# Kernel optimization log

Measured on AMD Instinct MI355X. Metric: run time of the kernel, lower is better.

The kernel has to match this reference:

```python
import jax, jax.numpy as jnp
import numpy as np

B, N, C = 2, 2048, 768
H, HD = 12, 64
HID = 3072
LN_EPS = 1e-5
POL_EPS = 1e-6


def _layer_norm(x, g, b):
    m = jnp.mean(x, axis=-1, keepdims=True)
    v = jnp.mean(jnp.square(x - m), axis=-1, keepdims=True)
    return (x - m) * jax.lax.rsqrt(v + LN_EPS) * g + b


def _softmax_with_policy(attn, policy):
    # attn: [B,H,N,N], policy: [B,N,1]
    n = attn.shape[-1]
    ap = policy.reshape(policy.shape[0], 1, 1, n)  # [B,1,1,N]
    eye = jnp.eye(n, dtype=ap.dtype)[None, None]   # [1,1,N,N]
    ap = ap + (1.0 - ap) * eye                     # always attend to self
    attn = attn - jnp.max(attn, axis=-1, keepdims=True)
    attn = jnp.exp(attn.astype(jnp.float32)) * ap.astype(jnp.float32)
    attn = (attn + POL_EPS / n) / (jnp.sum(attn, axis=-1, keepdims=True) + POL_EPS)
    return attn


def setup_inputs() -> dict:
    key = jax.random.key(0)
    ks = jax.random.split(key, 12)
    s = lambda fan_in: 1.0 / np.sqrt(fan_in)
    x = jax.random.normal(ks[0], (B, N, C), dtype=jnp.float32)
    policy = (jax.random.uniform(ks[1], (B, N, 1)) > 0.5).astype(jnp.float32)
    return {
        "x": x,
        "policy": policy,
        "ln1_g": jnp.ones((C,), jnp.float32),
        "ln1_b": jnp.zeros((C,), jnp.float32),
        "qkv_w": jax.random.uniform(ks[2], (3 * H * HD, C), jnp.float32, -s(C), s(C)),
        "proj_w": jax.random.uniform(ks[3], (C, H * HD), jnp.float32, -s(H * HD), s(H * HD)),
        "proj_b": jnp.zeros((C,), jnp.float32),
        "ln2_g": jnp.ones((C,), jnp.float32),
        "ln2_b": jnp.zeros((C,), jnp.float32),
        "fc1_w": jax.random.uniform(ks[4], (HID, C), jnp.float32, -s(C), s(C)),
        "fc1_b": jnp.zeros((HID,), jnp.float32),
        "fc2_w": jax.random.uniform(ks[5], (C, HID), jnp.float32, -s(HID), s(HID)),
        "fc2_b": jnp.zeros((C,), jnp.float32),
    }


def reference(x, policy, ln1_g, ln1_b, qkv_w, proj_w, proj_b, ln2_g, ln2_b, fc1_w, fc1_b, fc2_w, fc2_b):
    b, n, c = x.shape
    scale = HD ** -0.5
    # --- attention branch (pre-LN) ---
    h = _layer_norm(x, ln1_g, ln1_b)
    qkv = (h @ qkv_w.T).reshape(b, n, 3, H, HD).transpose(2, 0, 3, 1, 4)  # [3,B,H,N,hd]
    q, k, v = qkv[0], qkv[1], qkv[2]
    attn = jnp.einsum("bhqd,bhkd->bhqk", q * scale, k)
    attn = _softmax_with_policy(attn, policy).astype(x.dtype)
    o = jnp.einsum("bhqk,bhkd->bhqd", attn, v).transpose(0, 2, 1, 3).reshape(b, n, H * HD)
    x = x + (o @ proj_w.T + proj_b)  # skip_lam = 1.0, dropout/drop_path = identity
    # --- MLP branch (pre-LN) ---
    h = _layer_norm(x, ln2_g, ln2_b)
    h = jax.nn.gelu(h @ fc1_w.T + fc1_b, approximate=False)  # torch nn.GELU = exact erf
    x = x + (h @ fc2_w.T + fc2_b)
    return x
```

## Files before the change

kernel.cpp:

```cpp
#include <hip/hip_runtime.h>

typedef unsigned short u16;
typedef unsigned int u32;
typedef float f32x4 __attribute__((ext_vector_type(4)));
typedef float f32x16 __attribute__((ext_vector_type(16)));
typedef __bf16 bf16x8 __attribute__((ext_vector_type(8)));
typedef u16 u16x4v __attribute__((ext_vector_type(4)));
typedef u32 u32x2 __attribute__((ext_vector_type(2)));
typedef u32 u32x4 __attribute__((ext_vector_type(4)));

#define NHEAD 12
#define NN 2048
#define CC 768

#define GLOBAL_AS __attribute__((address_space(1)))
#define LDS_AS __attribute__((address_space(3)))

__device__ __forceinline__ u16 tobf(float f) {
  __bf16 h = (__bf16)f;
  return __builtin_bit_cast(u16, h);
}
__device__ __forceinline__ float bf2f(u16 h) {
  u32 u = ((u32)h) << 16;
  return __builtin_bit_cast(float, u);
}
__device__ __forceinline__ void plswap(u32& a, u32& b) {
  asm volatile("v_permlane32_swap_b32 %0, %1" : "+v"(a), "+v"(b));
}
__device__ __forceinline__ void plswapf(float& a, float& b) {
  asm volatile("v_permlane32_swap_b32 %0, %1" : "+v"(a), "+v"(b));
}

#define N4_QKV 442368
#define N4_PROJ 147456
#define N4_FC 589824
__global__ __launch_bounds__(256) void cvt4_kernel(
    const float* __restrict__ a, const float* __restrict__ b,
    const float* __restrict__ c, const float* __restrict__ d,
    u16* __restrict__ oa, u16* __restrict__ ob, u16* __restrict__ oc,
    u16* __restrict__ od) {
  int i = blockIdx.x * 256 + threadIdx.x;
  const float* src;
  u16* dst;
  if (i < N4_QKV) {
    src = a; dst = oa;
  } else if (i < N4_QKV + N4_PROJ) {
    i -= N4_QKV; src = b; dst = ob;
  } else if (i < N4_QKV + N4_PROJ + N4_FC) {
    i -= N4_QKV + N4_PROJ; src = c; dst = oc;
  } else {
    i -= N4_QKV + N4_PROJ + N4_FC; src = d; dst = od;
    if (i >= N4_FC) return;
  }
  float4 v = ((const float4*)src)[i];
  u16x4v o = {tobf(v.x), tobf(v.y), tobf(v.z), tobf(v.w)};
  ((u16x4v*)dst)[i] = o;
}

__global__ __launch_bounds__(256) void ln_kernel(const float* __restrict__ x,
                                                 const float* __restrict__ gw,
                                                 const float* __restrict__ bw,
                                                 u16* __restrict__ out) {
  int row = blockIdx.x * 4 + (threadIdx.x >> 6);
  int lane = threadIdx.x & 63;
  const float* xr = x + (size_t)row * CC + lane * 12;
  float v[12];
  *(float4*)&v[0] = *(const float4*)(xr + 0);
  *(float4*)&v[4] = *(const float4*)(xr + 4);
  *(float4*)&v[8] = *(const float4*)(xr + 8);
  float s = 0.f, sq = 0.f;
#pragma unroll
  for (int j = 0; j < 12; ++j) { s += v[j]; sq += v[j] * v[j]; }
#pragma unroll
  for (int o = 1; o < 64; o <<= 1) { s += __shfl_xor(s, o); sq += __shfl_xor(sq, o); }
  float mean = s * (1.f / CC);
  float var = sq * (1.f / CC) - mean * mean;
  float rs = rsqrtf(var + 1e-5f);
  u16 ob[12];
#pragma unroll
  for (int j = 0; j < 12; ++j) {
    int c = lane * 12 + j;
    ob[j] = tobf((v[j] - mean) * rs * gw[c] + bw[c]);
  }
  u32* orow = (u32*)(out + (size_t)row * CC + lane * 12);
#pragma unroll
  for (int j = 0; j < 6; ++j) orow[j] = (u32)ob[2 * j] | ((u32)ob[2 * j + 1] << 16);
}

template <int BM, int OB, int HASB, int ACT, int RES>
__global__ __launch_bounds__(256) void gemm_kernel(
    const u16* __restrict__ A, const u16* __restrict__ Bw,
    const float* __restrict__ bias, const float* __restrict__ res,
    void* __restrict__ Cout, int M, int N, int K) {
  constexpr int MW = BM / 2;
  constexpr int MF = MW / 16;
  __shared__ __align__(16) u16 Alds[BM * 64];
  __shared__ __align__(16) u16 Blds[128 * 64];
  const int tid = threadIdx.x;
  const int lane = tid & 63, wave = tid >> 6;
  const int l15 = lane & 15, g = lane >> 4;
  const int bm = blockIdx.x * BM, bn = blockIdx.y * 128;
  const int wm = (wave >> 1) * MW, wn = (wave & 1) * 64;
  f32x4 acc[MF][4] = {};

  for (int kt = 0; kt < K; kt += 64) {
#pragma unroll
    for (int i = 0; i < BM / 32; ++i) {
      int ob_ = i * 4096 + wave * 1024;
      int lb = ob_ + lane * 16;
      int row = lb >> 7;
      int cb = (lb & 127) ^ ((row & 7) << 4);
      const u16* sa = A + (size_t)(bm + row) * K + kt + (cb >> 1);
      __builtin_amdgcn_global_load_lds((const GLOBAL_AS void*)sa,
                                       (LDS_AS void*)(Alds + (ob_ >> 1)), 16, 0, 0);
    }
#pragma unroll
    for (int i = 0; i < 4; ++i) {
      int ob_ = i * 4096 + wave * 1024;
      int lb = ob_ + lane * 16;
      int row = lb >> 7;
      int cb = (lb & 127) ^ ((row & 7) << 4);
      const u16* sb = Bw + (size_t)(bn + row) * K + kt + (cb >> 1);
      __builtin_amdgcn_global_load_lds((const GLOBAL_AS void*)sb,
                                       (LDS_AS void*)(Blds + (ob_ >> 1)), 16, 0, 0);
    }
    __syncthreads();
#pragma unroll
    for (int ks = 0; ks < 2; ++ks) {
      bf16x8 af[MF], bfr[4];
#pragma unroll
      for (int mi = 0; mi < MF; ++mi) {
        int row = wm + mi * 16 + l15;
        int cb = (ks * 64 + g * 16) ^ ((row & 7) << 4);
        af[mi] = *(const bf16x8*)&Alds[row * 64 + (cb >> 1)];
      }
#pragma unroll
      for (int ni = 0; ni < 4; ++ni) {
        int row = wn + ni * 16 + l15;
        int cb = (ks * 64 + g * 16) ^ ((row & 7) << 4);
        bfr[ni] = *(const bf16x8*)&Blds[row * 64 + (cb >> 1)];
      }
#pragma unroll
      for (int mi = 0; mi < MF; ++mi)
#pragma unroll
        for (int ni = 0; ni < 4; ++ni)
          acc[mi][ni] = __builtin_amdgcn_mfma_f32_16x16x32_bf16(af[mi], bfr[ni],
                                                                acc[mi][ni], 0, 0, 0);
    }
    __syncthreads();
  }
#pragma unroll
  for (int mi = 0; mi < MF; ++mi) {
#pragma unroll
    for (int ni = 0; ni < 4; ++ni) {
      int col = bn + wn + ni * 16 + l15;
      float bs = HASB ? bias[col] : 0.f;
#pragma unroll
      for (int r = 0; r < 4; ++r) {
        int rowm = bm + wm + mi * 16 + g * 4 + r;
        float v = acc[mi][ni][r] + bs;
        if (ACT) v = 0.5f * v * (1.f + erff(v * 0.70710678118654752f));
        if (RES) v += res[(size_t)rowm * N + col];
        if (OB)
          ((u16*)Cout)[(size_t)rowm * N + col] = tobf(v);
        else
          ((float*)Cout)[(size_t)rowm * N + col] = v;
      }
    }
  }
}

__global__ __launch_bounds__(256) void vsum_kernel(const u16* __restrict__ qkv,
                                                   float* __restrict__ vs) {
  int bh = blockIdx.x, q4 = blockIdx.y;
  int b = bh / NHEAD, h = bh % NHEAD;
  int d = threadIdx.x & 63, part = threadIdx.x >> 6;
  float s = 0.f;
  for (int n = q4 * 512 + part; n < q4 * 512 + 512; n += 4)
    s += bf2f(qkv[(size_t)(b * NN + n) * 2304 + 2 * CC + h * 64 + d]);
  __shared__ float red[256];
  red[threadIdx.x] = s;
  __syncthreads();
  if (threadIdx.x < 64) {
    float t = red[threadIdx.x] + red[threadIdx.x + 64] + red[threadIdx.x + 128] +
              red[threadIdx.x + 192];
    vs[q4 * (24 * 64) + bh * 64 + threadIdx.x] = t;
  }
}

#define SCL2E 0.18033688f
#define TRRD(dst, addr, OFF) \
  asm volatile("ds_read_b64_tr_b16 %0, %1 offset:" OFF : "=v"(dst) : "v"(addr))

__global__ __launch_bounds__(256) void attn32_kernel(const u16* __restrict__ qkv,
                                                     const float* __restrict__ policy,
                                                     float* __restrict__ partO,
                                                     float* __restrict__ partlm) {
  __shared__ __align__(16) u16 Klds[2][4096];
  __shared__ __align__(16) u16 Vlds[2][4096];
  __shared__ u16 PolB[NN];
  __shared__ float alf[4][32];
  const int bh = blockIdx.y, b = bh / NHEAD, h = bh % NHEAD;
  const int qt = blockIdx.x >> 1, half = blockIdx.x & 1;
  const int tid = threadIdx.x, lane = tid & 63, w = tid >> 6;
  const int l31 = lane & 31, hp = lane >> 5, b4 = (lane >> 4) & 1;
  const int q0 = qt * 128 + w * 32;
  const int dv = q0 >> 6;
  const int ktd = (q0 >> 5) & 1;
  const int kv0 = half * 1024;
  const size_t adv = (size_t)64 * 2304;

  bf16x8 qf0, qf1, qf2, qf3;
  {
    const u16* qp = qkv + (size_t)(b * NN + q0 + l31) * 2304 + h * 64 + 8 * hp;
#pragma unroll
    for (int ds = 0; ds < 4; ++ds) {
      bf16x8 r = *(const bf16x8*)(qp + ds * 16);
      bf16x8 o;
#pragma unroll
      for (int j = 0; j < 8; ++j) o[j] = (__bf16)((float)r[j] * SCL2E);
      if (ds == 0) qf0 = o; else if (ds == 1) qf1 = o; else if (ds == 2) qf2 = o; else qf3 = o;
    }
  }

  const u16* ksrc[2];
  const u16* vsrcp[2];
#pragma unroll
  for (int c = 0; c < 2; ++c) {
    int lb = c * 4096 + w * 1024 + lane * 16;
    int row = lb >> 7;
    int cb = (lb & 127) ^ ((row & 7) << 4);
    ksrc[c] = qkv + (size_t)(b * NN + kv0 + row) * 2304 + CC + h * 64 + (cb >> 1);
    int idx0 = (c * 256 + w * 64 + lane) * 8;
    int s0 = idx0 & 15, jj = (idx0 >> 4) & 3, b4v = (idx0 >> 6) & 1,
        pv = (idx0 >> 7) & 1, hv = (idx0 >> 8) & 1, dtv = (idx0 >> 9) & 1,
        mkv = (idx0 >> 10) & 3;
    int key = mkv * 16 + 8 * hv + 4 * pv + jj;
    int d0 = dtv * 32 + 16 * b4v + s0;
    vsrcp[c] = qkv + (size_t)(b * NN + kv0 + key) * 2304 + 2 * CC + h * 64 + d0;
  }
  auto stage = [&](int buf) {
#pragma unroll
    for (int c = 0; c < 2; ++c) {
      __builtin_amdgcn_global_load_lds((const GLOBAL_AS void*)ksrc[c],
                                       (LDS_AS void*)&Klds[buf][c * 2048 + w * 512], 16, 0, 0);
      __builtin_amdgcn_global_load_lds((const GLOBAL_AS void*)vsrcp[c],
                                       (LDS_AS void*)&Vlds[buf][c * 2048 + w * 512], 16, 0, 0);
      ksrc[c] += adv; vsrcp[c] += adv;
    }
  };

  stage(0);
  {
    float4 p0 = *(const float4*)&policy[b * NN + tid * 8];
    float4 p1 = *(const float4*)&policy[b * NN + tid * 8 + 4];
    u16x4v a = {tobf(p0.x), tobf(p0.y), tobf(p0.z), tobf(p0.w)};
    u16x4v c2 = {tobf(p1.x), tobf(p1.y), tobf(p1.z), tobf(p1.w)};
    *(u16x4v*)&PolB[tid * 8] = a;
    *(u16x4v*)&PolB[tid * 8 + 4] = c2;
  }
  __syncthreads();

  float m_cur = -3.0e38f, m_true = -3.0e38f, l_run = 0.f;
  f32x16 accd[2] = {};
  const u32 vbase = (u32)(uintptr_t)(LDS_AS u16*)&Vlds[0][0] +
                    (u32)(2 * (lane & 15) + 128 * b4 + 512 * hp);

  for (int t = 0; t < 16; ++t) {
    const int cur = t & 1;
    const int kvg = kv0 + t * 64;
    if (t < 15) stage(cur ^ 1);

    f32x16 sv0, sv1;
    {
      bf16x8 kf[4];
#pragma unroll
      for (int ds = 0; ds < 4; ++ds) {
        int row = l31;
        int cb = (32 * ds + 16 * hp) ^ ((row & 7) << 4);
        kf[ds] = *(const bf16x8*)((const char*)&Klds[cur][0] + row * 128 + cb);
      }
      f32x16 a = {};
      a = __builtin_amdgcn_mfma_f32_32x32x16_bf16(kf[0], qf0, a, 0, 0, 0);
      a = __builtin_amdgcn_mfma_f32_32x32x16_bf16(kf[1], qf1, a, 0, 0, 0);
      a = __builtin_amdgcn_mfma_f32_32x32x16_bf16(kf[2], qf2, a, 0, 0, 0);
      a = __builtin_amdgcn_mfma_f32_32x32x16_bf16(kf[3], qf3, a, 0, 0, 0);
      sv0 = a;
    }
    {
      bf16x8 kf[4];
#pragma unroll
      for (int ds = 0; ds < 4; ++ds) {
        int row = 32 + l31;
        int cb = (32 * ds + 16 * hp) ^ ((row & 7) << 4);
        kf[ds] = *(const bf16x8*)((const char*)&Klds[cur][0] + row * 128 + cb);
      }
      f32x16 a = {};
      a = __builtin_amdgcn_mfma_f32_32x32x16_bf16(kf[0], qf0, a, 0, 0, 0);
      a = __builtin_amdgcn_mfma_f32_32x32x16_bf16(kf[1], qf1, a, 0, 0, 0);
      a = __builtin_amdgcn_mfma_f32_32x32x16_bf16(kf[2], qf2, a, 0, 0, 0);
      a = __builtin_amdgcn_mfma_f32_32x32x16_bf16(kf[3], qf3, a, 0, 0, 0);
      sv1 = a;
    }

    u32x2 tr[4][2][2];
    {
      u32 vab = vbase + (u32)(cur * 8192);
      TRRD(tr[0][0][0], vab, "0");    TRRD(tr[0][0][1], vab, "256");
      TRRD(tr[0][1][0], vab, "1024"); TRRD(tr[0][1][1], vab, "1280");
      TRRD(tr[1][0][0], vab, "2048"); TRRD(tr[1][0][1], vab, "2304");
      TRRD(tr[1][1][0], vab, "3072"); TRRD(tr[1][1][1], vab, "3328");
      TRRD(tr[2][0][0], vab, "4096"); TRRD(tr[2][0][1], vab, "4352");
      TRRD(tr[3][0][0], vab, "6144"); TRRD(tr[3][0][1], vab, "6400");
      TRRD(tr[2][1][0], vab, "5120"); TRRD(tr[2][1][1], vab, "5376");
      TRRD(tr[3][1][0], vab, "7168"); TRRD(tr[3][1][1], vab, "7424");
    }

    float tmax = sv0[0];
#pragma unroll
    for (int r = 1; r < 16; ++r) tmax = fmaxf(tmax, sv0[r]);
#pragma unroll
    for (int r = 0; r < 16; ++r) tmax = fmaxf(tmax, sv1[r]);
    {
      float t1 = tmax, t2 = tmax;
      plswapf(t1, t2);
      tmax = fmaxf(t1, t2);
    }
    m_true = fmaxf(m_true, tmax);
    const bool defer = __all(tmax <= m_cur + 8.f);
    const float m_new = defer ? m_cur : fmaxf(m_cur, tmax);

    const bool isdiag = ((half * 16 + t) == dv);
    u16 pb[32];
    float psum = 0.f;
#pragma unroll
    for (int kt = 0; kt < 2; ++kt) {
#pragma unroll
      for (int i = 0; i < 4; ++i) {
        u16x4v pq = *(const u16x4v*)&PolB[kvg + kt * 32 + 8 * i + 4 * hp];
#pragma unroll
        for (int rq = 0; rq < 4; ++rq) {
          int r = 4 * i + rq;
          float ap = bf2f(pq[rq]);
          if (isdiag && kt == ktd) ap = ((8 * i + 4 * hp + rq) == l31) ? 1.f : ap;
          float sval = kt ? sv1[r] : sv0[r];
          float e = exp2f(sval - m_new) * ap;
          u16 eb = tobf(e);
          psum += bf2f(eb);
          pb[kt * 16 + r] = eb;
        }
      }
    }
    {
      float s1 = psum, s2 = psum;
      plswapf(s1, s2);
      psum = s1 + s2;
    }
    if (!defer) {
      float alpha = exp2f(m_cur - m_new);
      l_run = l_run * alpha + psum;
      m_cur = m_new;
      if (lane < 32) alf[w][lane] = alpha;
      float4 aq0 = *(const float4*)&alf[w][4 * hp];
      float4 aq1 = *(const float4*)&alf[w][8 + 4 * hp];
      float4 aq2 = *(const float4*)&alf[w][16 + 4 * hp];
      float4 aq3 = *(const float4*)&alf[w][24 + 4 * hp];
#pragma unroll
      for (int dt = 0; dt < 2; ++dt) {
#pragma unroll
        for (int rq = 0; rq < 4; ++rq) {
          accd[dt][0 + rq] *= ((const float*)&aq0)[rq];
          accd[dt][4 + rq] *= ((const float*)&aq1)[rq];
          accd[dt][8 + rq] *= ((const float*)&aq2)[rq];
          accd[dt][12 + rq] *= ((const float*)&aq3)[rq];
        }
      }
    } else {
      l_run += psum;
    }

    u32 PK[4][4];
#pragma unroll
    for (int mk = 0; mk < 4; ++mk) {
      int bs = 16 * (mk >> 1) + 8 * (mk & 1);
      PK[mk][0] = (u32)pb[bs + 0] | ((u32)pb[bs + 1] << 16);
      PK[mk][1] = (u32)pb[bs + 2] | ((u32)pb[bs + 3] << 16);
      PK[mk][2] = (u32)pb[bs + 4] | ((u32)pb[bs + 5] << 16);
      PK[mk][3] = (u32)pb[bs + 6] | ((u32)pb[bs + 7] << 16);
      plswap(PK[mk][2], PK[mk][0]);
      plswap(PK[mk][3], PK[mk][1]);
    }

    asm volatile("s_waitcnt lgkmcnt(0)" ::: "memory");
    __builtin_amdgcn_sched_barrier(0);

#pragma unroll
    for (int mk = 0; mk < 4; ++mk) {
      u32x4 pk4 = {PK[mk][0], PK[mk][1], PK[mk][2], PK[mk][3]};
      bf16x8 pf = __builtin_bit_cast(bf16x8, pk4);
#pragma unroll
      for (int dt = 0; dt < 2; ++dt) {
        u32x4 vv = {tr[mk][dt][0].x, tr[mk][dt][0].y, tr[mk][dt][1].x, tr[mk][dt][1].y};
        bf16x8 vf = __builtin_bit_cast(bf16x8, vv);
        accd[dt] = __builtin_amdgcn_mfma_f32_32x32x16_bf16(pf, vf, accd[dt], 0, 0, 0);
      }
    }
    __syncthreads();
  }

  float sr = exp2f(m_cur - m_true);
  if (lane < 32) {
    alf[w][lane] = sr;
    float2 lm = {l_run * sr, m_true};
    *(float2*)&partlm[2 * ((size_t)(half * 24 + bh) * 2048 + q0 + lane)] = lm;
  }
  float4 sq0 = *(const float4*)&alf[w][4 * hp];
  float4 sq1 = *(const float4*)&alf[w][8 + 4 * hp];
  float4 sq2 = *(const float4*)&alf[w][16 + 4 * hp];
  float4 sq3 = *(const float4*)&alf[w][24 + 4 * hp];
  float* pb2 = partO + ((size_t)(half * 24 + bh) * 2048) * 64;
#pragma unroll
  for (int dt = 0; dt < 2; ++dt) {
#pragma unroll
    for (int i = 0; i < 4; ++i) {
      float4 sqv = (i == 0) ? sq0 : (i == 1) ? sq1 : (i == 2) ? sq2 : sq3;
#pragma unroll
      for (int rq = 0; rq < 4; ++rq) {
        int row = q0 + 8 * i + 4 * hp + rq;
        pb2[(size_t)row * 64 + dt * 32 + l31] = accd[dt][4 * i + rq] * ((const float*)&sqv)[rq];
      }
    }
  }
}

__global__ __launch_bounds__(256) void merge_kernel(const float* __restrict__ partO,
                                                    const float* __restrict__ partlm,
                                                    const float* __restrict__ vs,
                                                    u16* __restrict__ o) {
  int rr = blockIdx.x * 4 + (threadIdx.x >> 6);
  int lane = threadIdx.x & 63;
  int bh = rr >> 11, q = rr & 2047;
  int b = bh / NHEAD, h = bh % NHEAD;
  const float* O1 = partO + ((size_t)bh * 2048 + q) * 64;
  const float* O2 = partO + ((size_t)(24 + bh) * 2048 + q) * 64;
  float2 lm1 = ((const float2*)partlm)[(size_t)bh * 2048 + q];
  float2 lm2 = ((const float2*)partlm)[(size_t)(24 + bh) * 2048 + q];
  float ms = fmaxf(lm1.y, lm2.y);
  float w1 = exp2f(lm1.y - ms), w2 = exp2f(lm2.y - ms);
  float den = lm1.x * w1 + lm2.x * w2 + 1e-6f;
  float vsv = vs[bh * 64 + lane] + vs[1536 + bh * 64 + lane] +
              vs[3072 + bh * 64 + lane] + vs[4608 + bh * 64 + lane];
  float num = O1[lane] * w1 + O2[lane] * w2 + (1e-6f / 2048.f) * vsv;
  o[((size_t)(b * NN + q)) * CC + h * 64 + lane] = tobf(num / den);
}

extern "C" void kernel_launch(void* const* d_in, const int* in_sizes, int n_in,
                              void* d_out, int out_size, void* d_ws, size_t ws_size,
                              hipStream_t stream) {
  const float* x = (const float*)d_in[0];
  const float* policy = (const float*)d_in[1];
  const float* ln1g = (const float*)d_in[2];
  const float* ln1b = (const float*)d_in[3];
  const float* qkvw = (const float*)d_in[4];
  const float* projw = (const float*)d_in[5];
  const float* projb = (const float*)d_in[6];
  const float* ln2g = (const float*)d_in[7];
  const float* ln2b = (const float*)d_in[8];
  const float* fc1w = (const float*)d_in[9];
  const float* fc1b = (const float*)d_in[10];
  const float* fc2w = (const float*)d_in[11];
  const float* fc2b = (const float*)d_in[12];
  float* out = (float*)d_out;

  char* ws = (char*)d_ws;
  size_t off = 0;
  auto alloc = [&](size_t bytes) {
    void* p = ws + off;
    off = (off + bytes + 255) & ~(size_t)255;
    return p;
  };
  u16* wq = (u16*)alloc((size_t)2304 * 768 * 2);
  u16* wp = (u16*)alloc((size_t)768 * 768 * 2);
  u16* w1 = (u16*)alloc((size_t)3072 * 768 * 2);
  u16* w2 = (u16*)alloc((size_t)768 * 3072 * 2);
  u16* hbuf = (u16*)alloc((size_t)4096 * 768 * 2);
  u16* qkv = (u16*)alloc((size_t)4096 * 2304 * 2);
  u16* obuf = (u16*)alloc((size_t)4096 * 768 * 2);
  float* vs = (float*)alloc((size_t)4 * 24 * 64 * 4);
  size_t unionOff = off;
  float* partO = (float*)alloc((size_t)2 * 24 * 2048 * 64 * 4);
  float* partlm = (float*)alloc((size_t)2 * 24 * 2048 * 2 * 4);
  float* x1 = (float*)(ws + unionOff);
  u16* f1 = qkv;

  cvt4_kernel<<<6912, 256, 0, stream>>>(qkvw, projw, fc1w, fc2w, wq, wp, w1, w2);

  ln_kernel<<<1024, 256, 0, stream>>>(x, ln1g, ln1b, hbuf);
  gemm_kernel<128, 1, 0, 0, 0><<<dim3(32, 18), 256, 0, stream>>>(
      hbuf, wq, nullptr, nullptr, qkv, 4096, 2304, 768);
  vsum_kernel<<<dim3(24, 4), 256, 0, stream>>>(qkv, vs);
  attn32_kernel<<<dim3(32, 24), 256, 0, stream>>>(qkv, policy, partO, partlm);
  merge_kernel<<<12288, 256, 0, stream>>>(partO, partlm, vs, obuf);
  gemm_kernel<64, 0, 1, 0, 1><<<dim3(64, 6), 256, 0, stream>>>(
      obuf, wp, projb, x, x1, 4096, 768, 768);
  ln_kernel<<<1024, 256, 0, stream>>>(x1, ln2g, ln2b, hbuf);
  gemm_kernel<128, 1, 1, 1, 0><<<dim3(32, 24), 256, 0, stream>>>(
      hbuf, w1, fc1b, nullptr, f1, 4096, 3072, 768);
  gemm_kernel<64, 0, 1, 0, 1><<<dim3(64, 6), 256, 0, stream>>>(
      f1, w2, fc2b, x1, out, 4096, 768, 3072);
}
```

Measured before the change: 254.4 us.

## Load K directly to registers and give each wave private V buffers without block barriers

The attention kernel drops the shared K LDS tiles and loads each wave's K fragments straight from global memory into registers. V tiles go into per-wave LDS double buffers. Iteration moves to 32-key tiles, and explicit vmcnt waits replace the per-iteration __syncthreads. The aim is to remove block-wide synchronisation and LDS traffic for K, letting waves run independently with software-pipelined loads. The cost is that every wave now reads K separately from global memory, which adds redundant traffic, and each tile is smaller.

```diff
diff --git a/kernel.cpp b/kernel.cpp
--- a/kernel.cpp
+++ b/kernel.cpp
@@ -191,24 +191,23 @@
 #define SCL2E 0.18033688f
 #define TRRD(dst, addr, OFF) \
   asm volatile("ds_read_b64_tr_b16 %0, %1 offset:" OFF : "=v"(dst) : "v"(addr))
+#define VMW(N)                                          \
+  asm volatile("s_waitcnt vmcnt(" #N ")" ::: "memory"); \
+  __builtin_amdgcn_sched_barrier(0);
 
 __global__ __launch_bounds__(256) void attn32_kernel(const u16* __restrict__ qkv,
                                                      const float* __restrict__ policy,
                                                      float* __restrict__ partO,
                                                      float* __restrict__ partlm) {
-  __shared__ __align__(16) u16 Klds[2][4096];
-  __shared__ __align__(16) u16 Vlds[2][4096];
+  __shared__ __align__(16) u16 Vlds[4][2][2048];
   __shared__ u16 PolB[NN];
   __shared__ float alf[4][32];
   const int bh = blockIdx.y, b = bh / NHEAD, h = bh % NHEAD;
   const int qt = blockIdx.x >> 1, half = blockIdx.x & 1;
   const int tid = threadIdx.x, lane = tid & 63, w = tid >> 6;
-  const int l31 = lane & 31, hp = lane >> 5, b4 = (lane >> 4) & 1;
+  const int l31 = lane & 31, hp = lane >> 5, b4 = (lane >> 4) & 1, l15 = lane & 15;
   const int q0 = qt * 128 + w * 32;
-  const int dv = q0 >> 6;
-  const int ktd = (q0 >> 5) & 1;
   const int kv0 = half * 1024;
-  const size_t adv = (size_t)64 * 2304;
 
   bf16x8 qf0, qf1, qf2, qf3;
   {
@@ -223,34 +222,41 @@
     }
   }
 
-  const u16* ksrc[2];
-  const u16* vsrcp[2];
-#pragma unroll
-  for (int c = 0; c < 2; ++c) {
-    int lb = c * 4096 + w * 1024 + lane * 16;
-    int row = lb >> 7;
-    int cb = (lb & 127) ^ ((row & 7) << 4);
-    ksrc[c] = qkv + (size_t)(b * NN + kv0 + row) * 2304 + CC + h * 64 + (cb >> 1);
-    int idx0 = (c * 256 + w * 64 + lane) * 8;
+  const u16* kptr = qkv + (size_t)(b * NN + kv0 + l31) * 2304 + CC + h * 64 + 8 * hp;
+  const u16* vsrc[4];
+#pragma unroll
+  for (int c = 0; c < 4; ++c) {
+    int L = c * 64 + lane;
+    int idx0 = L * 8;
     int s0 = idx0 & 15, jj = (idx0 >> 4) & 3, b4v = (idx0 >> 6) & 1,
         pv = (idx0 >> 7) & 1, hv = (idx0 >> 8) & 1, dtv = (idx0 >> 9) & 1,
-        mkv = (idx0 >> 10) & 3;
+        mkv = (idx0 >> 10) & 1;
     int key = mkv * 16 + 8 * hv + 4 * pv + jj;
     int d0 = dtv * 32 + 16 * b4v + s0;
-    vsrcp[c] = qkv + (size_t)(b * NN + kv0 + key) * 2304 + 2 * CC + h * 64 + d0;
-  }
-  auto stage = [&](int buf) {
-#pragma unroll
-    for (int c = 0; c < 2; ++c) {
-      __builtin_amdgcn_global_load_lds((const GLOBAL_AS void*)ksrc[c],
-                                       (LDS_AS void*)&Klds[buf][c * 2048 + w * 512], 16, 0, 0);
-      __builtin_amdgcn_global_load_lds((const GLOBAL_AS void*)vsrcp[c],
-                                       (LDS_AS void*)&Vlds[buf][c * 2048 + w * 512], 16, 0, 0);
-      ksrc[c] += adv; vsrcp[c] += adv;
-    }
-  };
-
-  stage(0);
+    vsrc[c] = qkv + (size_t)(b * NN + kv0 + key) * 2304 + 2 * CC + h * 64 + d0;
+  }
+
+#define LOADK(R0, R1, R2, R3)              \
+  {                                        \
+    R0 = *(const bf16x8*)(kptr);           \
+    R1 = *(const bf16x8*)(kptr + 16);      \
+    R2 = *(const bf16x8*)(kptr + 32);      \
+    R3 = *(const bf16x8*)(kptr + 48);      \
+    kptr += 73728;                         \
+  }
+#define STAGEV(BUF)                                                              \
+  {                                                                              \
+    _Pragma("unroll") for (int c = 0; c < 4; ++c) {                              \
+      __builtin_amdgcn_global_load_lds((const GLOBAL_AS void*)vsrc[c],           \
+                                       (LDS_AS void*)&Vlds[w][BUF][c * 512], 16, \
+                                       0, 0);                                    \
+      vsrc[c] += 73728;                                                          \
+    }                                                                            \
+  }
+
+  bf16x8 kA0, kA1, kA2, kA3, kB0, kB1, kB2, kB3;
+  STAGEV(0);
+  LOADK(kA0, kA1, kA2, kA3);
   {
     float4 p0 = *(const float4*)&policy[b * NN + tid * 8];
     float4 p1 = *(const float4*)&policy[b * NN + tid * 8 + 4];
@@ -263,64 +269,32 @@
 
   float m_cur = -3.0e38f, m_true = -3.0e38f, l_run = 0.f;
   f32x16 accd[2] = {};
-  const u32 vbase = (u32)(uintptr_t)(LDS_AS u16*)&Vlds[0][0] +
-                    (u32)(2 * (lane & 15) + 128 * b4 + 512 * hp);
-
-  for (int t = 0; t < 16; ++t) {
-    const int cur = t & 1;
-    const int kvg = kv0 + t * 64;
-    if (t < 15) stage(cur ^ 1);
-
-    f32x16 sv0, sv1;
+  const u32 vwb = (u32)(uintptr_t)(LDS_AS u16*)&Vlds[w][0][0] +
+                  (u32)(2 * l15 + 128 * b4 + 512 * hp);
+
+  auto tile_body = [&](int T, bf16x8 k0, bf16x8 k1, bf16x8 k2, bf16x8 k3,
+                       int bufb) {
+    f32x16 sv = {};
+    sv = __builtin_amdgcn_mfma_f32_32x32x16_bf16(k0, qf0, sv, 0, 0, 0);
+    sv = __builtin_amdgcn_mfma_f32_32x32x16_bf16(k1, qf1, sv, 0, 0, 0);
+    sv = __builtin_amdgcn_mfma_f32_32x32x16_bf16(k2, qf2, sv, 0, 0, 0);
+    sv = __builtin_amdgcn_mfma_f32_32x32x16_bf16(k3, qf3, sv, 0, 0, 0);
+
+    u32x2 t00a, t00b, t01a, t01b, t10a, t10b, t11a, t11b;
     {
-      bf16x8 kf[4];
-#pragma unroll
-      for (int ds = 0; ds < 4; ++ds) {
-        int row = l31;
-        int cb = (32 * ds + 16 * hp) ^ ((row & 7) << 4);
-        kf[ds] = *(const bf16x8*)((const char*)&Klds[cur][0] + row * 128 + cb);
-      }
-      f32x16 a = {};
-      a = __builtin_amdgcn_mfma_f32_32x32x16_bf16(kf[0], qf0, a, 0, 0, 0);
-      a = __builtin_amdgcn_mfma_f32_32x32x16_bf16(kf[1], qf1, a, 0, 0, 0);
-      a = __builtin_amdgcn_mfma_f32_32x32x16_bf16(kf[2], qf2, a, 0, 0, 0);
-      a = __builtin_amdgcn_mfma_f32_32x32x16_bf16(kf[3], qf3, a, 0, 0, 0);
-      sv0 = a;
-    }
-    {
-      bf16x8 kf[4];
-#pragma unroll
-      for (int ds = 0; ds < 4; ++ds) {
-        int row = 32 + l31;
-        int cb = (32 * ds + 16 * hp) ^ ((row & 7) << 4);
-        kf[ds] = *(const bf16x8*)((const char*)&Klds[cur][0] + row * 128 + cb);
-      }
-      f32x16 a = {};
-      a = __builtin_amdgcn_mfma_f32_32x32x16_bf16(kf[0], qf0, a, 0, 0, 0);
-      a = __builtin_amdgcn_mfma_f32_32x32x16_bf16(kf[1], qf1, a, 0, 0, 0);
-      a = __builtin_amdgcn_mfma_f32_32x32x16_bf16(kf[2], qf2, a, 0, 0, 0);
-      a = __builtin_amdgcn_mfma_f32_32x32x16_bf16(kf[3], qf3, a, 0, 0, 0);
-      sv1 = a;
-    }
-
-    u32x2 tr[4][2][2];
-    {
-      u32 vab = vbase + (u32)(cur * 8192);
-      TRRD(tr[0][0][0], vab, "0");    TRRD(tr[0][0][1], vab, "256");
-      TRRD(tr[0][1][0], vab, "1024"); TRRD(tr[0][1][1], vab, "1280");
-      TRRD(tr[1][0][0], vab, "2048"); TRRD(tr[1][0][1], vab, "2304");
-      TRRD(tr[1][1][0], vab, "3072"); TRRD(tr[1][1][1], vab, "3328");
-      TRRD(tr[2][0][0], vab, "4096"); TRRD(tr[2][0][1], vab, "4352");
-      TRRD(tr[3][0][0], vab, "6144"); TRRD(tr[3][0][1], vab, "6400");
-      TRRD(tr[2][1][0], vab, "5120"); TRRD(tr[2][1][1], vab, "5376");
-      TRRD(tr[3][1][0], vab, "7168"); TRRD(tr[3][1][1], vab, "7424");
-    }
-
-    float tmax = sv0[0];
-#pragma unroll
-    for (int r = 1; r < 16; ++r) tmax = fmaxf(tmax, sv0[r]);
-#pragma unroll
-    for (int r = 0; r < 16; ++r) tmax = fmaxf(tmax, sv1[r]);
+      u32 vab = vwb + (u32)(bufb * 4096);
+      TRRD(t00a, vab, "0");    TRRD(t00b, vab, "256");
+      TRRD(t01a, vab, "1024"); TRRD(t01b, vab, "1280");
+      TRRD(t10a, vab, "2048"); TRRD(t10b, vab, "2304");
+      TRRD(t11a, vab, "3072"); TRRD(t11b, vab, "3328");
+    }
+
+    float m01 = fmaxf(sv[0], sv[1]), m23 = fmaxf(sv[2], sv[3]);
+    float m45 = fmaxf(sv[4], sv[5]), m67 = fmaxf(sv[6], sv[7]);
+    float m89 = fmaxf(sv[8], sv[9]), mab = fmaxf(sv[10], sv[11]);
+    float mcd = fmaxf(sv[12], sv[13]), mef = fmaxf(sv[14], sv[15]);
+    float tmax = fmaxf(fmaxf(fmaxf(m01, m23), fmaxf(m45, m67)),
+                       fmaxf(fmaxf(m89, mab), fmaxf(mcd, mef)));
     {
       float t1 = tmax, t2 = tmax;
       plswapf(t1, t2);
@@ -330,25 +304,22 @@
     const bool defer = __all(tmax <= m_cur + 8.f);
     const float m_new = defer ? m_cur : fmaxf(m_cur, tmax);
 
-    const bool isdiag = ((half * 16 + t) == dv);
-    u16 pb[32];
+    const int kvg = kv0 + T * 32;
+    const bool isdiag = (kvg == q0);
+    u16 pb[16];
     float psum = 0.f;
 #pragma unroll
-    for (int kt = 0; kt < 2; ++kt) {
-#pragma unroll
-      for (int i = 0; i < 4; ++i) {
-        u16x4v pq = *(const u16x4v*)&PolB[kvg + kt * 32 + 8 * i + 4 * hp];
-#pragma unroll
-        for (int rq = 0; rq < 4; ++rq) {
-          int r = 4 * i + rq;
-          float ap = bf2f(pq[rq]);
-          if (isdiag && kt == ktd) ap = ((8 * i + 4 * hp + rq) == l31) ? 1.f : ap;
-          float sval = kt ? sv1[r] : sv0[r];
-          float e = exp2f(sval - m_new) * ap;
-          u16 eb = tobf(e);
-          psum += bf2f(eb);
-          pb[kt * 16 + r] = eb;
-        }
+    for (int i = 0; i < 4; ++i) {
+      u16x4v pq = *(const u16x4v*)&PolB[kvg + 8 * i + 4 * hp];
+#pragma unroll
+      for (int rq = 0; rq < 4; ++rq) {
+        int r = 4 * i + rq;
+        float ap = bf2f(pq[rq]);
+        if (isdiag) ap = ((8 * i + 4 * hp + rq) == l31) ? 1.f : ap;
+        float e = exp2f(sv[r] - m_new) * ap;
+        u16 eb = tobf(e);
+        psum += bf2f(eb);
+        pb[r] = eb;
       }
     }
     {
@@ -379,33 +350,58 @@
       l_run += psum;
     }
 
-    u32 PK[4][4];
-#pragma unroll
-    for (int mk = 0; mk < 4; ++mk) {
-      int bs = 16 * (mk >> 1) + 8 * (mk & 1);
-      PK[mk][0] = (u32)pb[bs + 0] | ((u32)pb[bs + 1] << 16);
-      PK[mk][1] = (u32)pb[bs + 2] | ((u32)pb[bs + 3] << 16);
-      PK[mk][2] = (u32)pb[bs + 4] | ((u32)pb[bs + 5] << 16);
-      PK[mk][3] = (u32)pb[bs + 6] | ((u32)pb[bs + 7] << 16);
-      plswap(PK[mk][2], PK[mk][0]);
-      plswap(PK[mk][3], PK[mk][1]);
-    }
+    u32 PK0[4], PK1[4];
+    PK0[0] = (u32)pb[0] | ((u32)pb[1] << 16);
+    PK0[1] = (u32)pb[2] | ((u32)pb[3] << 16);
+    PK0[2] = (u32)pb[4] | ((u32)pb[5] << 16);
+    PK0[3] = (u32)pb[6] | ((u32)pb[7] << 16);
+    PK1[0] = (u32)pb[8] | ((u32)pb[9] << 16);
+    PK1[1] = (u32)pb[10] | ((u32)pb[11] << 16);
+    PK1[2] = (u32)pb[12] | ((u32)pb[13] << 16);
+    PK1[3] = (u32)pb[14] | ((u32)pb[15] << 16);
+    plswap(PK0[2], PK0[0]);
+    plswap(PK0[3], PK0[1]);
+    plswap(PK1[2], PK1[0]);
+    plswap(PK1[3], PK1[1]);
 
     asm volatile("s_waitcnt lgkmcnt(0)" ::: "memory");
     __builtin_amdgcn_sched_barrier(0);
 
-#pragma unroll
-    for (int mk = 0; mk < 4; ++mk) {
-      u32x4 pk4 = {PK[mk][0], PK[mk][1], PK[mk][2], PK[mk][3]};
-      bf16x8 pf = __builtin_bit_cast(bf16x8, pk4);
-#pragma unroll
-      for (int dt = 0; dt < 2; ++dt) {
-        u32x4 vv = {tr[mk][dt][0].x, tr[mk][dt][0].y, tr[mk][dt][1].x, tr[mk][dt][1].y};
-        bf16x8 vf = __builtin_bit_cast(bf16x8, vv);
-        accd[dt] = __builtin_amdgcn_mfma_f32_32x32x16_bf16(pf, vf, accd[dt], 0, 0, 0);
-      }
-    }
-    __syncthreads();
+    {
+      u32x4 p4 = {PK0[0], PK0[1], PK0[2], PK0[3]};
+      bf16x8 pf = __builtin_bit_cast(bf16x8, p4);
+      u32x4 v0 = {t00a.x, t00a.y, t00b.x, t00b.y};
+      u32x4 v1 = {t01a.x, t01a.y, t01b.x, t01b.y};
+      accd[0] = __builtin_amdgcn_mfma_f32_32x32x16_bf16(
+          pf, __builtin_bit_cast(bf16x8, v0), accd[0], 0, 0, 0);
+      accd[1] = __builtin_amdgcn_mfma_f32_32x32x16_bf16(
+          pf, __builtin_bit_cast(bf16x8, v1), accd[1], 0, 0, 0);
+    }
+    {
+      u32x4 p4 = {PK1[0], PK1[1], PK1[2], PK1[3]};
+      bf16x8 pf = __builtin_bit_cast(bf16x8, p4);
+      u32x4 v0 = {t10a.x, t10a.y, t10b.x, t10b.y};
+      u32x4 v1 = {t11a.x, t11a.y, t11b.x, t11b.y};
+      accd[0] = __builtin_amdgcn_mfma_f32_32x32x16_bf16(
+          pf, __builtin_bit_cast(bf16x8, v0), accd[0], 0, 0, 0);
+      accd[1] = __builtin_amdgcn_mfma_f32_32x32x16_bf16(
+          pf, __builtin_bit_cast(bf16x8, v1), accd[1], 0, 0, 0);
+    }
+  };
+
+  for (int tt = 0; tt < 16; ++tt) {
+    LOADK(kB0, kB1, kB2, kB3);
+    STAGEV(1);
+    VMW(8);
+    tile_body(2 * tt, kA0, kA1, kA2, kA3, 0);
+    if (tt < 15) {
+      LOADK(kA0, kA1, kA2, kA3);
+      STAGEV(0);
+      VMW(8);
+    } else {
+      VMW(0);
+    }
+    tile_body(2 * tt + 1, kB0, kB1, kB2, kB3, 1);
   }
 
   float sr = exp2f(m_cur - m_true);
@@ -431,6 +427,8 @@
       }
     }
   }
+#undef LOADK
+#undef STAGEV
 }
 
 __global__ __launch_bounds__(256) void merge_kernel(const float* __restrict__ partO,
```

After: 263.8 us. +3.7%, slower.
